# Performance work log

Hardware: AMD Instinct MI355X
Metric: run time of the kernel (lower is better)

Reference implementation:

```python
import jax, jax.numpy as jnp
import numpy as np

C_LEN, Q_LEN, D = 8192, 1024, 1024  # D = 2*hidden_size


def setup_inputs() -> dict:
    key = jax.random.key(0)
    ks = jax.random.split(key, 5)
    scale = 1.0 / np.sqrt(D)
    return {
        "H": jax.random.normal(ks[0], (C_LEN, D), dtype=jnp.float32),
        "U": jax.random.normal(ks[1], (Q_LEN, D), dtype=jnp.float32),
        "w_q": jax.random.normal(ks[2], (D,), dtype=jnp.float32) * scale,
        "b_q": jnp.zeros((1,), dtype=jnp.float32),
        "w_c": jax.random.normal(ks[3], (D,), dtype=jnp.float32) * scale,
        "b_c": jnp.zeros((1,), dtype=jnp.float32),
        "w_qc": jax.random.normal(ks[4], (D,), dtype=jnp.float32) * scale,
        "b_qc": jnp.zeros((1,), dtype=jnp.float32),
    }


def reference(H, U, w_q, b_q, w_c, b_c, w_qc, b_qc):
    # Per-token loop qc[:, i] = (H * U[i]) @ w_qc + b_qc collapses to one GEMM:
    # qc[j, i] = sum_k H[j,k] * w_qc[k] * U[i,k] + b_qc
    qc = jnp.einsum("cd,qd->cq", H * w_qc, U) + b_qc          # [c_len, q_len]
    q_term = (U @ w_q + b_q)[None, :]                          # [1, q_len]
    c_term = (H @ w_c + b_c)[:, None]                          # [c_len, 1]
    s = qc + q_term + c_term                                    # [c_len, q_len]
    q2c_atten = jax.nn.softmax(s, axis=0)                       # softmax over context dim (as written)
    U_toggler = q2c_atten @ U                                   # [c_len, D]
    b = jnp.max(H, axis=1)                                      # [c_len]
    c2q_atten = jax.nn.softmax(b)                               # [c_len]
    H_toggler = jnp.broadcast_to((c2q_atten @ H)[None, :], (H.shape[0], H.shape[1]))
    return (U_toggler, H_toggler)
```

## Files before the change

kernel.cpp:

```cpp
#include <hip/hip_runtime.h>

#define C_LEN 8192
#define Q_LEN 1024
#define DDIM  1024

typedef __attribute__((ext_vector_type(8))) short short8;
typedef __attribute__((ext_vector_type(4))) float f32x4;

static __device__ __forceinline__ unsigned short f2bf(float f){
  unsigned u = __float_as_uint(f);
  unsigned rounding = 0x7fffu + ((u >> 16) & 1u);
  return (unsigned short)((u + rounding) >> 16);
}
static __device__ __forceinline__ float bf2f(unsigned short b){
  return __uint_as_float(((unsigned)b) << 16);
}

static __device__ __forceinline__ void async_copy16(const void* g, void* l){
  __builtin_amdgcn_global_load_lds(
      (const __attribute__((address_space(1))) void*)g,
      (__attribute__((address_space(3))) void*)l, 16, 0, 0);
}

static __device__ __forceinline__ float waveRedSum(float v){
  #pragma unroll
  for(int o=32;o;o>>=1) v += __shfl_down(v,o);
  return v;
}
static __device__ __forceinline__ float waveRedMax(float v){
  #pragma unroll
  for(int o=32;o;o>>=1) v = fmaxf(v,__shfl_down(v,o));
  return v;
}

__global__ void prep_H(const float* __restrict__ H, const float* __restrict__ w_qc,
                       const float* __restrict__ w_c, const float* __restrict__ b_c,
                       unsigned short* __restrict__ Abf, float* __restrict__ c_term,
                       float* __restrict__ eb){
  const int c = blockIdx.x, t = threadIdx.x;
  float4 h   = reinterpret_cast<const float4*>(H + (size_t)c*DDIM)[t];
  float4 wqc = reinterpret_cast<const float4*>(w_qc)[t];
  float4 wc  = reinterpret_cast<const float4*>(w_c)[t];
  float dot = h.x*wc.x + h.y*wc.y + h.z*wc.z + h.w*wc.w;
  float mx  = fmaxf(fmaxf(h.x,h.y), fmaxf(h.z,h.w));
  ushort4 o;
  o.x=f2bf(h.x*wqc.x); o.y=f2bf(h.y*wqc.y); o.z=f2bf(h.z*wqc.z); o.w=f2bf(h.w*wqc.w);
  reinterpret_cast<ushort4*>(Abf)[(size_t)c*256 + t] = o;
  __shared__ float sd[4], sm[4];
  int w=t>>6, l=t&63;
  dot = waveRedSum(dot); mx = waveRedMax(mx);
  if(l==0){ sd[w]=dot; sm[w]=mx; }
  __syncthreads();
  if(t==0){
    c_term[c] = sd[0]+sd[1]+sd[2]+sd[3] + b_c[0];
    float m = fmaxf(fmaxf(sm[0],sm[1]), fmaxf(sm[2],sm[3]));
    eb[c] = __expf(m);
  }
}

__global__ void sum_eb(const float* __restrict__ eb, float* __restrict__ btot){
  __shared__ float red[16];
  int t = threadIdx.x, w = t>>6, l = t&63;
  float s = eb[t] + eb[t + 1024] + eb[t + 2048] + eb[t + 3072]
          + eb[t + 4096] + eb[t + 5120] + eb[t + 6144] + eb[t + 7168];
  s = waveRedSum(s);
  if(!l) red[w] = s;
  __syncthreads();
  if(t==0){ float tot=0.f; for(int i=0;i<16;i++) tot+=red[i]; btot[0]=tot; }
}

__global__ void prep_U(const float* __restrict__ U, const float* __restrict__ w_q,
                       const float* __restrict__ b_q, unsigned short* __restrict__ Ubf,
                       float* __restrict__ q_term){
  const int qr = blockIdx.x, t = threadIdx.x;
  float4 u  = reinterpret_cast<const float4*>(U + (size_t)qr*DDIM)[t];
  float4 wq = reinterpret_cast<const float4*>(w_q)[t];
  float dot = u.x*wq.x + u.y*wq.y + u.z*wq.z + u.w*wq.w;
  ushort4 o; o.x=f2bf(u.x); o.y=f2bf(u.y); o.z=f2bf(u.z); o.w=f2bf(u.w);
  reinterpret_cast<ushort4*>(Ubf)[(size_t)qr*256 + t] = o;
  __shared__ float sd[4];
  int w=t>>6, l=t&63;
  dot = waveRedSum(dot);
  if(l==0) sd[w]=dot;
  __syncthreads();
  if(t==0) q_term[qr] = sd[0]+sd[1]+sd[2]+sd[3] + b_q[0];
}

__global__ void transpose_U(const float* __restrict__ U, unsigned short* __restrict__ Ut){
  __shared__ float tile[64][65];
  const int t = threadIdx.x;
  const int q0 = blockIdx.y*64, d0 = blockIdx.x*64;
  #pragma unroll
  for(int i=0;i<16;i++){
    int idx = i*256 + t, r = idx>>6, col = idx&63;
    tile[r][col] = U[(size_t)(q0+r)*DDIM + d0 + col];
  }
  __syncthreads();
  #pragma unroll
  for(int i=0;i<16;i++){
    int idx = i*256 + t, r = idx>>6, col = idx&63;
    Ut[(size_t)(d0+r)*Q_LEN + q0 + col] = f2bf(tile[col][r]);
  }
}

template<int FUSE_EXP>
__global__ __launch_bounds__(256)
void gemm_bt(const unsigned short* __restrict__ A, const unsigned short* __restrict__ B,
             void* __restrict__ Cout, int M, int N, int K,
             const float* __restrict__ rowAdd, const float* __restrict__ colAdd,
             const float* __restrict__ addC, float* __restrict__ csum){
  __shared__ unsigned short As[128][32];
  __shared__ unsigned short Bs[128][32];
  const int t = threadIdx.x;
  const int lane = t & 63, wave = t >> 6;
  const int wm = wave & 1, wn = wave >> 1;
  const int lr = lane & 15, quad = lane >> 4;
  const int bm = blockIdx.x * 128, bn = blockIdx.y * 128;
  const int srow = wave*32 + (lane>>2);
  const int skcol = (lane&3)*8;

  f32x4 acc[4][4];
  #pragma unroll
  for(int i=0;i<4;i++)
    #pragma unroll
    for(int j=0;j<4;j++) acc[i][j] = (f32x4){0.f,0.f,0.f,0.f};

  const unsigned short* gA = A + (size_t)(bm + srow)*K + skcol;
  const unsigned short* gB = B + (size_t)(bn + srow)*K + skcol;
  unsigned short* lA0 = &As[srow][skcol];
  unsigned short* lA1 = &As[srow+16][skcol];
  unsigned short* lB0 = &Bs[srow][skcol];
  unsigned short* lB1 = &Bs[srow+16][skcol];

  for(int k0=0;k0<K;k0+=32){
    async_copy16(gA,                lA0);
    async_copy16(gA + (size_t)16*K, lA1);
    async_copy16(gB,                lB0);
    async_copy16(gB + (size_t)16*K, lB1);
    gA += 32; gB += 32;
    __syncthreads();
    short8 af[4], bfr[4];
    #pragma unroll
    for(int i=0;i<4;i++){
      af[i]  = *reinterpret_cast<const short8*>(&As[wm*64 + i*16 + lr][quad*8]);
      bfr[i] = *reinterpret_cast<const short8*>(&Bs[wn*64 + i*16 + lr][quad*8]);
    }
    #pragma unroll
    for(int i=0;i<4;i++)
      #pragma unroll
      for(int j=0;j<4;j++)
        acc[i][j] = __builtin_amdgcn_mfma_f32_16x16x32_bf16(af[i], bfr[j], acc[i][j], 0,0,0);
    __syncthreads();
  }

  const int col0 = bn + wn*64;
  if(FUSE_EXP){
    unsigned short* P = (unsigned short*)Cout;
    const float ac = addC[0];
    float cs[4];
    #pragma unroll
    for(int j=0;j<4;j++) cs[j] = 0.f;
    #pragma unroll
    for(int i=0;i<4;i++){
      int row0 = bm + wm*64 + i*16 + quad*4;
      float ra0 = rowAdd[row0], ra1 = rowAdd[row0+1], ra2 = rowAdd[row0+2], ra3 = rowAdd[row0+3];
      #pragma unroll
      for(int j=0;j<4;j++){
        int col = col0 + j*16 + lr;
        float cadd = colAdd[col] + ac;
        float e0 = __expf(acc[i][j][0] + ra0 + cadd);
        float e1 = __expf(acc[i][j][1] + ra1 + cadd);
        float e2 = __expf(acc[i][j][2] + ra2 + cadd);
        float e3 = __expf(acc[i][j][3] + ra3 + cadd);
        P[(size_t)(row0  )*N + col] = f2bf(e0);
        P[(size_t)(row0+1)*N + col] = f2bf(e1);
        P[(size_t)(row0+2)*N + col] = f2bf(e2);
        P[(size_t)(row0+3)*N + col] = f2bf(e3);
        cs[j] += e0+e1+e2+e3;
      }
    }
    #pragma unroll
    for(int j=0;j<4;j++){
      float v = cs[j];
      v += __shfl_xor(v, 16);
      v += __shfl_xor(v, 32);
      if(quad==0) atomicAdd(&csum[col0 + j*16 + lr], v);
    }
  } else {
    float* C = (float*)Cout;
    #pragma unroll
    for(int i=0;i<4;i++){
      int row0 = bm + wm*64 + i*16 + quad*4;
      #pragma unroll
      for(int j=0;j<4;j++){
        int col = col0 + j*16 + lr;
        #pragma unroll
        for(int r=0;r<4;r++)
          C[(size_t)(row0+r)*N + col] = acc[i][j][r];
      }
    }
  }
}

__global__ void scale_Ut(unsigned short* __restrict__ Ut, const float* __restrict__ csum){
  int idx = blockIdx.x*256 + threadIdx.x;
  int q = idx & (Q_LEN-1);
  Ut[idx] = f2bf(bf2f(Ut[idx]) / csum[q]);
}

__global__ void h_weighted(const float* __restrict__ H, const float* __restrict__ eb,
                           float* __restrict__ Hrow){
  int d  = blockIdx.x*256 + threadIdx.x;
  int c0 = blockIdx.y*256;
  float acc = 0.f;
  for(int c=c0;c<c0+256;c++)
    acc += eb[c] * H[(size_t)c*DDIM + d];
  atomicAdd(&Hrow[d], acc);
}

__global__ void bcast_H(const float* __restrict__ Hrow, const float* __restrict__ btot,
                        float4* __restrict__ out4){
  int gid = blockIdx.x*256 + threadIdx.x;
  int d4 = gid & 255;
  float inv = 1.f / btot[0];
  float4 v = reinterpret_cast<const float4*>(Hrow)[d4];
  v.x*=inv; v.y*=inv; v.z*=inv; v.w*=inv;
  out4[gid] = v;
}

extern "C" void kernel_launch(void* const* d_in, const int* in_sizes, int n_in,
                              void* d_out, int out_size, void* d_ws, size_t ws_size,
                              hipStream_t stream){
  const float* H    = (const float*)d_in[0];
  const float* U    = (const float*)d_in[1];
  const float* w_q  = (const float*)d_in[2];
  const float* b_q  = (const float*)d_in[3];
  const float* w_c  = (const float*)d_in[4];
  const float* b_c  = (const float*)d_in[5];
  const float* w_qc = (const float*)d_in[6];
  const float* b_qc = (const float*)d_in[7];
  float* out = (float*)d_out;
  char*  ws  = (char*)d_ws;

  unsigned short* P    = (unsigned short*)(ws);
  unsigned short* Abf  = (unsigned short*)(ws + 16777216);
  unsigned short* Ubf  = (unsigned short*)(ws + 33554432);
  unsigned short* Utb  = (unsigned short*)(ws + 35651584);
  char* stats = ws + 37748736;
  float* csum  = (float*)(stats);
  float* Hrow  = (float*)(stats + 4096);
  float* btot  = (float*)(stats + 8192);
  float* cterm = (float*)(stats + 12288);
  float* eb    = (float*)(stats + 45056);
  float* qterm = (float*)(stats + 77824);

  hipMemsetAsync(stats, 0, 8192, stream);

  prep_H<<<C_LEN, 256, 0, stream>>>(H, w_qc, w_c, b_c, Abf, cterm, eb);
  prep_U<<<Q_LEN, 256, 0, stream>>>(U, w_q, b_q, Ubf, qterm);
  transpose_U<<<dim3(16,16), 256, 0, stream>>>(U, Utb);

  gemm_bt<1><<<dim3(64,8), 256, 0, stream>>>(Abf, Ubf, (void*)P, C_LEN, Q_LEN, DDIM,
                                             cterm, qterm, b_qc, csum);

  scale_Ut<<<4096, 256, 0, stream>>>(Utb, csum);

  gemm_bt<0><<<dim3(64,8), 256, 0, stream>>>(P, Utb, (void*)out, C_LEN, DDIM, Q_LEN,
                                             nullptr, nullptr, nullptr, nullptr);

  sum_eb    <<<1, 1024, 0, stream>>>(eb, btot);
  h_weighted<<<dim3(4,32), 256, 0, stream>>>(H, eb, Hrow);
  bcast_H   <<<8192, 256, 0, stream>>>(Hrow, btot, (float4*)(out + (size_t)C_LEN*DDIM));
}
```

Baseline: 192.1 us.

## Double-buffer GEMM LDS tiles and fuse softmax scaling into U transpose

The bf16 GEMM now uses two LDS buffers, issuing the async global-to-LDS load for the next K tile before computing on the current one. This removes one barrier per iteration and lets loads overlap the MFMA work. The separate scale_Ut pass is folded into the transpose kernel, which now runs after the first GEMM and multiplies by the reciprocal column sum. The 1/btot normalisation moves into h_weighted so the broadcast is a plain copy. LDS use doubles, and the pipeline relies on the barrier waiting for the async loads.

```diff
diff --git a/kernel.cpp b/kernel.cpp
--- a/kernel.cpp
+++ b/kernel.cpp
@@ -11,9 +11,6 @@
   unsigned u = __float_as_uint(f);
   unsigned rounding = 0x7fffu + ((u >> 16) & 1u);
   return (unsigned short)((u + rounding) >> 16);
-}
-static __device__ __forceinline__ float bf2f(unsigned short b){
-  return __uint_as_float(((unsigned)b) << 16);
 }
 
 static __device__ __forceinline__ void async_copy16(const void* g, void* l){
@@ -86,7 +83,8 @@
   if(t==0) q_term[qr] = sd[0]+sd[1]+sd[2]+sd[3] + b_q[0];
 }
 
-__global__ void transpose_U(const float* __restrict__ U, unsigned short* __restrict__ Ut){
+__global__ void transpose_scale_U(const float* __restrict__ U, const float* __restrict__ csum,
+                                  unsigned short* __restrict__ Ut){
   __shared__ float tile[64][65];
   const int t = threadIdx.x;
   const int q0 = blockIdx.y*64, d0 = blockIdx.x*64;
@@ -95,11 +93,12 @@
     int idx = i*256 + t, r = idx>>6, col = idx&63;
     tile[r][col] = U[(size_t)(q0+r)*DDIM + d0 + col];
   }
+  float inv = 1.f / csum[q0 + (t&63)];
   __syncthreads();
   #pragma unroll
   for(int i=0;i<16;i++){
     int idx = i*256 + t, r = idx>>6, col = idx&63;
-    Ut[(size_t)(d0+r)*Q_LEN + q0 + col] = f2bf(tile[col][r]);
+    Ut[(size_t)(d0+r)*Q_LEN + q0 + col] = f2bf(tile[col][r] * inv);
   }
 }
 
@@ -109,8 +108,8 @@
              void* __restrict__ Cout, int M, int N, int K,
              const float* __restrict__ rowAdd, const float* __restrict__ colAdd,
              const float* __restrict__ addC, float* __restrict__ csum){
-  __shared__ unsigned short As[128][32];
-  __shared__ unsigned short Bs[128][32];
+  __shared__ unsigned short As[2][128][32];
+  __shared__ unsigned short Bs[2][128][32];
   const int t = threadIdx.x;
   const int lane = t & 63, wave = t >> 6;
   const int wm = wave & 1, wn = wave >> 1;
@@ -127,30 +126,37 @@
 
   const unsigned short* gA = A + (size_t)(bm + srow)*K + skcol;
   const unsigned short* gB = B + (size_t)(bn + srow)*K + skcol;
-  unsigned short* lA0 = &As[srow][skcol];
-  unsigned short* lA1 = &As[srow+16][skcol];
-  unsigned short* lB0 = &Bs[srow][skcol];
-  unsigned short* lB1 = &Bs[srow+16][skcol];
-
-  for(int k0=0;k0<K;k0+=32){
-    async_copy16(gA,                lA0);
-    async_copy16(gA + (size_t)16*K, lA1);
-    async_copy16(gB,                lB0);
-    async_copy16(gB + (size_t)16*K, lB1);
-    gA += 32; gB += 32;
+  unsigned short* lA[2] = { &As[0][srow][skcol], &As[1][srow][skcol] };
+  unsigned short* lB[2] = { &Bs[0][srow][skcol], &Bs[1][srow][skcol] };
+
+  async_copy16(gA,                lA[0]);
+  async_copy16(gA + (size_t)16*K, lA[0] + 16*32);
+  async_copy16(gB,                lB[0]);
+  async_copy16(gB + (size_t)16*K, lB[0] + 16*32);
+  gA += 32; gB += 32;
+
+  const int ITERS = K >> 5;
+  for(int k=0;k<ITERS;k++){
+    const int cur = k & 1, nxt = cur ^ 1;
     __syncthreads();
+    if(k+1 < ITERS){
+      async_copy16(gA,                lA[nxt]);
+      async_copy16(gA + (size_t)16*K, lA[nxt] + 16*32);
+      async_copy16(gB,                lB[nxt]);
+      async_copy16(gB + (size_t)16*K, lB[nxt] + 16*32);
+      gA += 32; gB += 32;
+    }
     short8 af[4], bfr[4];
     #pragma unroll
     for(int i=0;i<4;i++){
-      af[i]  = *reinterpret_cast<const short8*>(&As[wm*64 + i*16 + lr][quad*8]);
-      bfr[i] = *reinterpret_cast<const short8*>(&Bs[wn*64 + i*16 + lr][quad*8]);
+      af[i]  = *reinterpret_cast<const short8*>(&As[cur][wm*64 + i*16 + lr][quad*8]);
+      bfr[i] = *reinterpret_cast<const short8*>(&Bs[cur][wn*64 + i*16 + lr][quad*8]);
     }
     #pragma unroll
     for(int i=0;i<4;i++)
       #pragma unroll
       for(int j=0;j<4;j++)
         acc[i][j] = __builtin_amdgcn_mfma_f32_16x16x32_bf16(af[i], bfr[j], acc[i][j], 0,0,0);
-    __syncthreads();
   }
 
   const int col0 = bn + wn*64;
@@ -202,30 +208,20 @@
   }
 }
 
-__global__ void scale_Ut(unsigned short* __restrict__ Ut, const float* __restrict__ csum){
-  int idx = blockIdx.x*256 + threadIdx.x;
-  int q = idx & (Q_LEN-1);
-  Ut[idx] = f2bf(bf2f(Ut[idx]) / csum[q]);
-}
-
 __global__ void h_weighted(const float* __restrict__ H, const float* __restrict__ eb,
-                           float* __restrict__ Hrow){
+                           const float* __restrict__ btot, float* __restrict__ Hrow){
   int d  = blockIdx.x*256 + threadIdx.x;
   int c0 = blockIdx.y*256;
   float acc = 0.f;
   for(int c=c0;c<c0+256;c++)
     acc += eb[c] * H[(size_t)c*DDIM + d];
-  atomicAdd(&Hrow[d], acc);
-}
-
-__global__ void bcast_H(const float* __restrict__ Hrow, const float* __restrict__ btot,
-                        float4* __restrict__ out4){
+  atomicAdd(&Hrow[d], acc * (1.f/btot[0]));
+}
+
+__global__ void bcast_H(const float* __restrict__ Hrow, float4* __restrict__ out4){
   int gid = blockIdx.x*256 + threadIdx.x;
   int d4 = gid & 255;
-  float inv = 1.f / btot[0];
-  float4 v = reinterpret_cast<const float4*>(Hrow)[d4];
-  v.x*=inv; v.y*=inv; v.z*=inv; v.w*=inv;
-  out4[gid] = v;
+  out4[gid] = reinterpret_cast<const float4*>(Hrow)[d4];
 }
 
 extern "C" void kernel_launch(void* const* d_in, const int* in_sizes, int n_in,
@@ -258,17 +254,16 @@
 
   prep_H<<<C_LEN, 256, 0, stream>>>(H, w_qc, w_c, b_c, Abf, cterm, eb);
   prep_U<<<Q_LEN, 256, 0, stream>>>(U, w_q, b_q, Ubf, qterm);
-  transpose_U<<<dim3(16,16), 256, 0, stream>>>(U, Utb);
 
   gemm_bt<1><<<dim3(64,8), 256, 0, stream>>>(Abf, Ubf, (void*)P, C_LEN, Q_LEN, DDIM,
                                              cterm, qterm, b_qc, csum);
 
-  scale_Ut<<<4096, 256, 0, stream>>>(Utb, csum);
+  transpose_scale_U<<<dim3(16,16), 256, 0, stream>>>(U, csum, Utb);
 
   gemm_bt<0><<<dim3(64,8), 256, 0, stream>>>(P, Utb, (void*)out, C_LEN, DDIM, Q_LEN,
                                              nullptr, nullptr, nullptr, nullptr);
 
   sum_eb    <<<1, 1024, 0, stream>>>(eb, btot);
-  h_weighted<<<dim3(4,32), 256, 0, stream>>>(H, eb, Hrow);
-  bcast_H   <<<8192, 256, 0, stream>>>(Hrow, btot, (float4*)(out + (size_t)C_LEN*DDIM));
-}
+  h_weighted<<<dim3(4,32), 256, 0, stream>>>(H, eb, btot, Hrow);
+  bcast_H   <<<8192, 256, 0, stream>>>(Hrow, (float4*)(out + (size_t)C_LEN*DDIM));
+}
```

New measurement: 177.0 us. 7.9% less time.
